# Performance work log

Hardware: AMD Instinct MI355X
Metric: run time of the kernel (lower is better)

The kernel has to match this reference:

```python
import jax, jax.numpy as jnp
import numpy as np

DIM = 1024
HEADS = 16
DIM_HEAD = 64


def setup_inputs() -> dict:
    key = jax.random.key(0)
    ks = jax.random.split(key, 6)
    b, n = 2, 2048
    x = jax.random.normal(ks[0], (b, n, DIM), dtype=jnp.float32)
    gamma = jnp.ones((DIM,), dtype=jnp.float32)
    w_qkv = jax.random.normal(ks[1], (DIM, 3 * HEADS * DIM_HEAD), dtype=jnp.float32) * (DIM ** -0.5)
    w_gates = jax.random.normal(ks[2], (DIM, HEADS), dtype=jnp.float32) * (DIM ** -0.5)
    b_gates = jnp.zeros((HEADS,), dtype=jnp.float32)
    w_out = jax.random.normal(ks[3], (HEADS * DIM_HEAD, DIM), dtype=jnp.float32) * ((HEADS * DIM_HEAD) ** -0.5)
    freqs = jax.random.uniform(ks[4], (DIM_HEAD // 2,), dtype=jnp.float32)
    return {"x": x, "gamma": gamma, "w_qkv": w_qkv, "w_gates": w_gates,
            "b_gates": b_gates, "w_out": w_out, "freqs": freqs}


def _rotate_half(t):
    # interleaved pairs: (x1, x2) -> (-x2, x1)
    tp = t.reshape(t.shape[:-1] + (t.shape[-1] // 2, 2))
    x1, x2 = tp[..., 0], tp[..., 1]
    return jnp.stack((-x2, x1), axis=-1).reshape(t.shape)


def reference(x, gamma, w_qkv, w_gates, b_gates, w_out, freqs):
    b, n, d = x.shape
    # RMSNorm variant: divide by L2 norm, scale by gamma * sqrt(dim)
    xn = x / jnp.linalg.norm(x, axis=-1, keepdims=True)
    xn = xn * gamma * (d ** 0.5)
    # QKV projection: (b, n, 3*H*D) -> q,k,v each (b, h, n, dh)
    qkv = xn @ w_qkv
    qkv = qkv.reshape(b, n, 3, HEADS, DIM_HEAD).transpose(2, 0, 3, 1, 4)
    q, k, v = qkv[0], qkv[1], qkv[2]
    # Inline RoPE (interleaved): freqs (n, dh)
    pos = jnp.arange(n, dtype=freqs.dtype)
    f = jnp.repeat(pos[:, None] * freqs[None, :], 2, axis=-1)  # (n, dh)
    cos_f, sin_f = jnp.cos(f), jnp.sin(f)
    q = q * cos_f + _rotate_half(q) * sin_f
    k = k * cos_f + _rotate_half(k) * sin_f
    # SDPA
    scale = DIM_HEAD ** -0.5
    scores = jnp.einsum('bhqd,bhkd->bhqk', q, k) * scale
    attn = jax.nn.softmax(scores, axis=-1)
    out = jnp.einsum('bhqk,bhkd->bhqd', attn, v)  # (b, h, n, dh)
    # per-head sigmoid gate from normalized input
    gates = xn @ w_gates + b_gates  # (b, n, h)
    out = out * jax.nn.sigmoid(gates.transpose(0, 2, 1))[..., None]
    # merge heads and output projection
    out = out.transpose(0, 2, 1, 3).reshape(b, n, HEADS * DIM_HEAD)
    return out @ w_out
```

## Files before the change

kernel.cpp:

```cpp
#include <hip/hip_runtime.h>

typedef __bf16 bf16_t;
typedef __bf16 bf16x8 __attribute__((ext_vector_type(8)));
typedef __bf16 bf16x4 __attribute__((ext_vector_type(4)));
typedef float f32x4 __attribute__((ext_vector_type(4)));

#define B_  2
#define N_  2048
#define D_  1024
#define H_  16
#define DH_ 64

#define QSCALE 0.18033688011112042f
#define NEGC  -11.541560327111707f

#if __has_builtin(__builtin_amdgcn_exp2f)
#define EXP2F(x) __builtin_amdgcn_exp2f(x)
#else
#define EXP2F(x) exp2f(x)
#endif

#define GLL16(g, l) __builtin_amdgcn_global_load_lds( \
    (const __attribute__((address_space(1))) void*)(g), \
    (__attribute__((address_space(3))) void*)(l), 16, 0, 0)

__device__ __forceinline__ int xcd_swizzle_id() {
  int id = blockIdx.y * gridDim.x + blockIdx.x;
  int cpx = (gridDim.x * gridDim.y) >> 3;
  return (id & 7) * cpx + (id >> 3);
}

__global__ __launch_bounds__(256) void k_rmsnorm_gates(const float* __restrict__ x,
    const float* __restrict__ gamma, const float* __restrict__ wg,
    const float* __restrict__ bg, bf16_t* __restrict__ xn, float* __restrict__ gsig) {
  int row = blockIdx.x;
  const float4* xr = (const float4*)(x + (size_t)row * D_);
  int tid = threadIdx.x;
  float4 v = xr[tid];
  float ss = v.x*v.x + v.y*v.y + v.z*v.z + v.w*v.w;
  #pragma unroll
  for (int off = 32; off > 0; off >>= 1) ss += __shfl_down(ss, off);
  __shared__ float red4[4];
  if ((tid & 63) == 0) red4[tid >> 6] = ss;
  __syncthreads();
  float scale = 32.0f * rsqrtf(red4[0] + red4[1] + red4[2] + red4[3]);
  float4 g = ((const float4*)gamma)[tid];
  bf16x4 o;
  o[0] = (bf16_t)(v.x * scale * g.x);
  o[1] = (bf16_t)(v.y * scale * g.y);
  o[2] = (bf16_t)(v.z * scale * g.z);
  o[3] = (bf16_t)(v.w * scale * g.w);
  *(bf16x4*)(xn + (size_t)row * D_ + tid * 4) = o;
  float xv[4] = {(float)o[0], (float)o[1], (float)o[2], (float)o[3]};
  float part[16];
  #pragma unroll
  for (int h = 0; h < 16; ++h) part[h] = 0.f;
  #pragma unroll
  for (int j = 0; j < 4; ++j) {
    const float4* wr = (const float4*)&wg[(size_t)(tid * 4 + j) * 16];
    #pragma unroll
    for (int q = 0; q < 4; ++q) {
      float4 w4 = wr[q];
      part[q * 4 + 0] += xv[j] * w4.x;
      part[q * 4 + 1] += xv[j] * w4.y;
      part[q * 4 + 2] += xv[j] * w4.z;
      part[q * 4 + 3] += xv[j] * w4.w;
    }
  }
  __shared__ float red[256][17];
  #pragma unroll
  for (int h = 0; h < 16; ++h) red[tid][h] = part[h];
  __syncthreads();
  int h = tid & 15, grp = tid >> 4;
  float s = 0.f;
  #pragma unroll
  for (int k = 0; k < 16; ++k) s += red[grp * 16 + k][h];
  __syncthreads();
  red[grp][h] = s;
  __syncthreads();
  if (tid < 16) {
    float acc = bg[tid];
    #pragma unroll
    for (int k = 0; k < 16; ++k) acc += red[k][tid];
    gsig[(size_t)row * 16 + tid] = 1.0f / (1.0f + __expf(-acc));
  }
}

__global__ __launch_bounds__(256) void k_transpose_cvt(const float* __restrict__ W,
    bf16_t* __restrict__ Wt, int R, int C) {
  __shared__ float tile[32][33];
  int c0 = blockIdx.x * 32, r0 = blockIdx.y * 32;
  int tx = threadIdx.x & 31, ty = threadIdx.x >> 5;
  #pragma unroll
  for (int i = 0; i < 4; ++i) {
    int r = ty + i * 8;
    tile[r][tx] = W[(size_t)(r0 + r) * C + c0 + tx];
  }
  __syncthreads();
  #pragma unroll
  for (int i = 0; i < 4; ++i) {
    int rr = ty + i * 8;
    Wt[(size_t)(c0 + rr) * R + r0 + tx] = (bf16_t)tile[tx][rr];
  }
}

template<bool OUT_BF16>
__global__ __launch_bounds__(256) void k_gemm_bt(const bf16_t* __restrict__ A,
    const bf16_t* __restrict__ Bt, void* __restrict__ Cp, int M, int N, int K) {
  constexpr int BK = 32;
  __shared__ __align__(16) bf16_t As[128 * BK];
  __shared__ __align__(16) bf16_t Bs[128 * BK];
  int tid = threadIdx.x, wave = tid >> 6, lane = tid & 63;
  int l16 = lane & 15, quad = lane >> 4;
  int swz = xcd_swizzle_id();
  int bxi = swz % gridDim.x, byi = swz / gridDim.x;
  int bm = bxi * 128, bn = byi * 128;
  int wm = (wave >> 1) * 64, wn = (wave & 1) * 64;
  int srow = wave * 32 + (lane >> 2);
  int scol = (lane & 3) * 8;
  const bf16_t* gA0 = &A [(size_t)(bm + srow)      * K + scol];
  const bf16_t* gA1 = &A [(size_t)(bm + srow + 16) * K + scol];
  const bf16_t* gB0 = &Bt[(size_t)(bn + srow)      * K + scol];
  const bf16_t* gB1 = &Bt[(size_t)(bn + srow + 16) * K + scol];
  bf16_t* lA0 = &As[(wave * 32)      * BK];
  bf16_t* lA1 = &As[(wave * 32 + 16) * BK];
  bf16_t* lB0 = &Bs[(wave * 32)      * BK];
  bf16_t* lB1 = &Bs[(wave * 32 + 16) * BK];
  f32x4 acc[4][4] = {};
  for (int k0 = 0; k0 < K; k0 += BK) {
    GLL16(gA0 + k0, lA0);
    GLL16(gA1 + k0, lA1);
    GLL16(gB0 + k0, lB0);
    GLL16(gB1 + k0, lB1);
    __syncthreads();
    bf16x8 af[4], bfr[4];
    #pragma unroll
    for (int t = 0; t < 4; ++t) {
      af[t]  = *(const bf16x8*)&As[(wm + t * 16 + l16) * BK + quad * 8];
      bfr[t] = *(const bf16x8*)&Bs[(wn + t * 16 + l16) * BK + quad * 8];
    }
    #pragma unroll
    for (int mt = 0; mt < 4; ++mt)
      #pragma unroll
      for (int nt = 0; nt < 4; ++nt)
        acc[mt][nt] = __builtin_amdgcn_mfma_f32_16x16x32_bf16(af[mt], bfr[nt], acc[mt][nt], 0, 0, 0);
    __syncthreads();
  }
  #pragma unroll
  for (int mt = 0; mt < 4; ++mt)
    #pragma unroll
    for (int nt = 0; nt < 4; ++nt)
      #pragma unroll
      for (int r = 0; r < 4; ++r) {
        int row = bm + wm + mt * 16 + quad * 4 + r;
        int col = bn + wn + nt * 16 + l16;
        float v = acc[mt][nt][r];
        if (OUT_BF16) ((bf16_t*)Cp)[(size_t)row * N + col] = (bf16_t)v;
        else          ((float*)Cp)[(size_t)row * N + col] = v;
      }
}

__global__ __launch_bounds__(256) void k_gemm_bt_n64(const bf16_t* __restrict__ A,
    const bf16_t* __restrict__ Bt, float* __restrict__ C, int M, int N, int K) {
  constexpr int BK = 32;
  __shared__ __align__(16) bf16_t As[128 * BK];
  __shared__ __align__(16) bf16_t Bs[64 * BK];
  int tid = threadIdx.x, wave = tid >> 6, lane = tid & 63;
  int l16 = lane & 15, quad = lane >> 4;
  int swz = xcd_swizzle_id();
  int bxi = swz % gridDim.x, byi = swz / gridDim.x;
  int bm = bxi * 128, bn = byi * 64;
  int wm = (wave >> 1) * 64, wn = (wave & 1) * 32;
  int srow = wave * 32 + (lane >> 2);
  int scol = (lane & 3) * 8;
  const bf16_t* gA0 = &A [(size_t)(bm + srow)      * K + scol];
  const bf16_t* gA1 = &A [(size_t)(bm + srow + 16) * K + scol];
  int srB = wave * 16 + (lane >> 2);
  const bf16_t* gB0 = &Bt[(size_t)(bn + srB) * K + scol];
  bf16_t* lA0 = &As[(wave * 32)      * BK];
  bf16_t* lA1 = &As[(wave * 32 + 16) * BK];
  bf16_t* lB0 = &Bs[(wave * 16)      * BK];
  f32x4 acc[4][2] = {};
  for (int k0 = 0; k0 < K; k0 += BK) {
    GLL16(gA0 + k0, lA0);
    GLL16(gA1 + k0, lA1);
    GLL16(gB0 + k0, lB0);
    __syncthreads();
    bf16x8 af[4], bfr[2];
    #pragma unroll
    for (int t = 0; t < 4; ++t)
      af[t]  = *(const bf16x8*)&As[(wm + t * 16 + l16) * BK + quad * 8];
    #pragma unroll
    for (int t = 0; t < 2; ++t)
      bfr[t] = *(const bf16x8*)&Bs[(wn + t * 16 + l16) * BK + quad * 8];
    #pragma unroll
    for (int mt = 0; mt < 4; ++mt)
      #pragma unroll
      for (int nt = 0; nt < 2; ++nt)
        acc[mt][nt] = __builtin_amdgcn_mfma_f32_16x16x32_bf16(af[mt], bfr[nt], acc[mt][nt], 0, 0, 0);
    __syncthreads();
  }
  #pragma unroll
  for (int mt = 0; mt < 4; ++mt)
    #pragma unroll
    for (int nt = 0; nt < 2; ++nt)
      #pragma unroll
      for (int r = 0; r < 4; ++r) {
        int row = bm + wm + mt * 16 + quad * 4 + r;
        int col = bn + wn + nt * 16 + l16;
        C[(size_t)row * N + col] = acc[mt][nt][r];
      }
}

__global__ __launch_bounds__(256) void k_rope(const bf16_t* __restrict__ qkvb,
    const float* __restrict__ freqs, bf16_t* __restrict__ Qb, bf16_t* __restrict__ Kb) {
  int row = blockIdx.x, b = row >> 11, n = row & 2047;
  __shared__ float cs[32], sn[32];
  int tid = threadIdx.x;
  if (tid < 32) { float f = (float)n * freqs[tid]; cs[tid] = cosf(f); sn[tid] = sinf(f); }
  __syncthreads();
  const bf16_t* src = qkvb + (size_t)row * 3072;
  int isK = tid >> 7;
  int t = tid & 127;
  int h = t >> 3, j8 = (t & 7) * 8;
  bf16x8 v = *(const bf16x8*)&src[isK * 1024 + h * 64 + j8];
  float qs = isK ? 1.0f : QSCALE;
  bf16x8 o;
  #pragma unroll
  for (int i = 0; i < 4; ++i) {
    int jj = (j8 >> 1) + i;
    float c = cs[jj], s = sn[jj];
    float v0 = (float)v[2 * i], v1 = (float)v[2 * i + 1];
    o[2 * i]     = (bf16_t)((v0 * c - v1 * s) * qs);
    o[2 * i + 1] = (bf16_t)((v1 * c + v0 * s) * qs);
  }
  bf16_t* dst = (isK ? Kb : Qb) + ((size_t)(b * H_ + h) * N_ + n) * DH_ + j8;
  *(bf16x8*)dst = o;
}

__global__ __launch_bounds__(256) void k_vtrans(const bf16_t* __restrict__ qkvb,
    bf16_t* __restrict__ Vb) {
  __shared__ bf16_t Vs[64][72];
  int bh = blockIdx.x, nt = blockIdx.y;
  int b = bh >> 4, h = bh & 15;
  int n0 = nt * 64;
  int tid = threadIdx.x;
  #pragma unroll
  for (int it = 0; it < 2; ++it) {
    int chunk = tid + 256 * it;
    int nl = chunk >> 3, c = (chunk & 7) * 8;
    *(bf16x8*)&Vs[nl][c] =
        *(const bf16x8*)&qkvb[(size_t)(b * N_ + n0 + nl) * 3072 + 2048 + h * 64 + c];
  }
  __syncthreads();
  #pragma unroll
  for (int it = 0; it < 2; ++it) {
    int chunk = tid + 256 * it;
    int d = chunk >> 3, nc = (chunk & 7) * 8;
    bf16x8 o;
    #pragma unroll
    for (int jj = 0; jj < 8; ++jj) o[jj] = Vs[nc + jj][d];
    *(bf16x8*)&Vb[((size_t)bh * DH_ + d) * N_ + n0 + nc] = o;
  }
}

__global__ __launch_bounds__(256) void k_flash(const bf16_t* __restrict__ Qb,
    const bf16_t* __restrict__ Kb, const bf16_t* __restrict__ Vb,
    const float* __restrict__ gsig, bf16_t* __restrict__ Ao) {
  __shared__ __align__(16) bf16_t Ks[2][64 * 72];
  __shared__ __align__(16) bf16_t Vt[2][64 * 72];
  __shared__ __align__(16) bf16_t Ps[4][32 * 72];
  int swz = xcd_swizzle_id();
  int qblk = swz & 15, bh = swz >> 4;
  int b = bh >> 4, h = bh & 15;
  int tid = threadIdx.x, wave = tid >> 6, lane = tid & 63;
  int l16 = lane & 15, quad = lane >> 4;
  int qw = qblk * 128 + wave * 32;
  const bf16_t* Qh = Qb + (size_t)bh * N_ * DH_;
  const bf16_t* Kh = Kb + (size_t)bh * N_ * DH_;
  const bf16_t* Vh = Vb + (size_t)bh * DH_ * N_;
  bf16_t* Pw = Ps[wave];
  bf16x8 qf[2][2];
  #pragma unroll
  for (int qt = 0; qt < 2; ++qt)
    #pragma unroll
    for (int hf = 0; hf < 2; ++hf)
      qf[qt][hf] = *(const bf16x8*)&Qh[(size_t)(qw + qt * 16 + l16) * DH_ + hf * 32 + quad * 8];
  bf16x8 onesf;
  #pragma unroll
  for (int i = 0; i < 8; ++i) onesf[i] = (bf16_t)1.0f;
  f32x4 accO[2][4] = {};
  f32x4 accL[2] = {};
  int sk = tid >> 3;
  int sc = (tid & 7) * 8;
  bf16x8 rk0 = *(const bf16x8*)&Kh[(size_t)sk * DH_ + sc];
  bf16x8 rk1 = *(const bf16x8*)&Kh[(size_t)(sk + 32) * DH_ + sc];
  bf16x8 rv0 = *(const bf16x8*)&Vh[(size_t)sk * N_ + sc];
  bf16x8 rv1 = *(const bf16x8*)&Vh[(size_t)(sk + 32) * N_ + sc];
  *(bf16x8*)&Ks[0][sk * 72 + sc]        = rk0;
  *(bf16x8*)&Ks[0][(sk + 32) * 72 + sc] = rk1;
  *(bf16x8*)&Vt[0][sk * 72 + sc]        = rv0;
  *(bf16x8*)&Vt[0][(sk + 32) * 72 + sc] = rv1;
  __syncthreads();
  const f32x4 zinit = {NEGC, NEGC, NEGC, NEGC};
  for (int k0 = 0; k0 < N_; k0 += 64) {
    int cur = (k0 >> 6) & 1;
    const bf16_t* Kc = Ks[cur];
    const bf16_t* Vc = Vt[cur];
    int kn = k0 + 64;
    if (kn < N_) {
      rk0 = *(const bf16x8*)&Kh[(size_t)(kn + sk) * DH_ + sc];
      rk1 = *(const bf16x8*)&Kh[(size_t)(kn + sk + 32) * DH_ + sc];
      rv0 = *(const bf16x8*)&Vh[(size_t)sk * N_ + kn + sc];
      rv1 = *(const bf16x8*)&Vh[(size_t)(sk + 32) * N_ + kn + sc];
    }
    f32x4 st[4][2];
    __builtin_amdgcn_s_setprio(1);
    #pragma unroll
    for (int kt = 0; kt < 4; ++kt) {
      bf16x8 kf0 = *(const bf16x8*)&Kc[(kt * 16 + l16) * 72 + quad * 8];
      bf16x8 kf1 = *(const bf16x8*)&Kc[(kt * 16 + l16) * 72 + 32 + quad * 8];
      #pragma unroll
      for (int qt = 0; qt < 2; ++qt) {
        f32x4 z = zinit;
        z = __builtin_amdgcn_mfma_f32_16x16x32_bf16(kf0, qf[qt][0], z, 0, 0, 0);
        z = __builtin_amdgcn_mfma_f32_16x16x32_bf16(kf1, qf[qt][1], z, 0, 0, 0);
        st[kt][qt] = z;
      }
    }
    __builtin_amdgcn_s_setprio(0);
    #pragma unroll
    for (int qt = 0; qt < 2; ++qt)
      #pragma unroll
      for (int kt = 0; kt < 4; ++kt) {
        bf16x4 pk;
        #pragma unroll
        for (int r = 0; r < 4; ++r)
          pk[r] = (bf16_t)EXP2F(st[kt][qt][r]);
        *(bf16x4*)&Pw[(qt * 16 + l16) * 72 + kt * 16 + quad * 4] = pk;
      }
    bf16x8 pf[2][2];
    #pragma unroll
    for (int qt = 0; qt < 2; ++qt)
      #pragma unroll
      for (int hf = 0; hf < 2; ++hf)
        pf[qt][hf] = *(const bf16x8*)&Pw[(qt * 16 + l16) * 72 + hf * 32 + quad * 8];
    __builtin_amdgcn_s_setprio(1);
    #pragma unroll
    for (int qt = 0; qt < 2; ++qt) {
      accL[qt] = __builtin_amdgcn_mfma_f32_16x16x32_bf16(pf[qt][0], onesf, accL[qt], 0, 0, 0);
      accL[qt] = __builtin_amdgcn_mfma_f32_16x16x32_bf16(pf[qt][1], onesf, accL[qt], 0, 0, 0);
    }
    #pragma unroll
    for (int dt = 0; dt < 4; ++dt)
      #pragma unroll
      for (int hf = 0; hf < 2; ++hf) {
        bf16x8 vf = *(const bf16x8*)&Vc[(dt * 16 + l16) * 72 + hf * 32 + quad * 8];
        #pragma unroll
        for (int qt = 0; qt < 2; ++qt)
          accO[qt][dt] = __builtin_amdgcn_mfma_f32_16x16x32_bf16(pf[qt][hf], vf, accO[qt][dt], 0, 0, 0);
      }
    __builtin_amdgcn_s_setprio(0);
    if (kn < N_) {
      int nb = cur ^ 1;
      *(bf16x8*)&Ks[nb][sk * 72 + sc]        = rk0;
      *(bf16x8*)&Ks[nb][(sk + 32) * 72 + sc] = rk1;
      *(bf16x8*)&Vt[nb][sk * 72 + sc]        = rv0;
      *(bf16x8*)&Vt[nb][(sk + 32) * 72 + sc] = rv1;
    }
    __syncthreads();
  }
  #pragma unroll
  for (int qt = 0; qt < 2; ++qt)
    #pragma unroll
    for (int r = 0; r < 4; ++r) {
      int q = qw + qt * 16 + quad * 4 + r;
      float g = gsig[((size_t)b * N_ + q) * H_ + h];
      float ginv = g / accL[qt][r];
      #pragma unroll
      for (int dt = 0; dt < 4; ++dt)
        Ao[((size_t)b * N_ + q) * (H_ * DH_) + h * DH_ + dt * 16 + l16] =
            (bf16_t)(accO[qt][dt][r] * ginv);
    }
}

extern "C" void kernel_launch(void* const* d_in, const int* in_sizes, int n_in,
                              void* d_out, int out_size, void* d_ws, size_t ws_size,
                              hipStream_t stream) {
  (void)in_sizes; (void)n_in; (void)out_size; (void)ws_size;
  const float* x      = (const float*)d_in[0];
  const float* gamma  = (const float*)d_in[1];
  const float* w_qkv  = (const float*)d_in[2];
  const float* w_gate = (const float*)d_in[3];
  const float* b_gate = (const float*)d_in[4];
  const float* w_out  = (const float*)d_in[5];
  const float* freqs  = (const float*)d_in[6];
  float* out = (float*)d_out;
  char* ws = (char*)d_ws;
  bf16_t* xn    = (bf16_t*)(ws);
  bf16_t* wqkvT = (bf16_t*)(ws + ((size_t)8  << 20));
  bf16_t* woutT = (bf16_t*)(ws + ((size_t)14 << 20));
  bf16_t* Qb    = (bf16_t*)(ws + ((size_t)16 << 20));
  bf16_t* Kb    = (bf16_t*)(ws + ((size_t)24 << 20));
  bf16_t* Vb    = (bf16_t*)(ws + ((size_t)32 << 20));
  float*  gsig  = (float*) (ws + ((size_t)40 << 20));
  bf16_t* attn  = (bf16_t*)(ws + ((size_t)41 << 20));
  bf16_t* qkvb  = (bf16_t*)(ws + ((size_t)49 << 20));

  k_transpose_cvt<<<dim3(3072 / 32, 1024 / 32), 256, 0, stream>>>(w_qkv, wqkvT, 1024, 3072);
  k_transpose_cvt<<<dim3(1024 / 32, 1024 / 32), 256, 0, stream>>>(w_out, woutT, 1024, 1024);
  k_rmsnorm_gates<<<4096, 256, 0, stream>>>(x, gamma, w_gate, b_gate, xn, gsig);
  k_gemm_bt<true><<<dim3(32, 24), 256, 0, stream>>>(xn, wqkvT, (void*)qkvb, 4096, 3072, 1024);
  k_rope<<<4096, 256, 0, stream>>>(qkvb, freqs, Qb, Kb);
  k_vtrans<<<dim3(32, 32), 256, 0, stream>>>(qkvb, Vb);
  k_flash<<<dim3(16, 32), 256, 0, stream>>>(Qb, Kb, Vb, gsig, attn);
  k_gemm_bt_n64<<<dim3(32, 16), 256, 0, stream>>>(attn, woutT, out, 4096, 1024, 1024);
}
```

Measured before the change: 239.2 us.

## Fuse RoPE and V transpose into QKV GEMM epilogue

Replaces the generic QKV GEMM plus separate rope and V-transpose kernels with one GEMM whose epilogue applies interleaved RoPE (using a lane shuffle to reach the partner element), scales Q, and writes Q/K in head-major layout and V transposed. A small kernel precomputes the cos/sin tables once per call. This removes the round-trip of the bf16 qkv intermediate through global memory and two launches. The price is scattered 2-byte stores for Q/K and 8-byte strided stores for V in the epilogue, which may coalesce poorly.

Result: no change. 242.4 us (+1.3%).

```diff
diff --git a/kernel.cpp b/kernel.cpp
--- a/kernel.cpp
+++ b/kernel.cpp
@@ -28,6 +28,15 @@
   int id = blockIdx.y * gridDim.x + blockIdx.x;
   int cpx = (gridDim.x * gridDim.y) >> 3;
   return (id & 7) * cpx + (id >> 3);
+}
+
+__global__ __launch_bounds__(256) void k_trig(const float* __restrict__ freqs,
+    float* __restrict__ tc, float* __restrict__ ts) {
+  int idx = blockIdx.x * 256 + threadIdx.x;
+  int n = idx >> 5, j = idx & 31;
+  float f = (float)n * freqs[j];
+  tc[idx] = cosf(f);
+  ts[idx] = sinf(f);
 }
 
 __global__ __launch_bounds__(256) void k_rmsnorm_gates(const float* __restrict__ x,
@@ -104,16 +113,17 @@
   }
 }
 
-template<bool OUT_BF16>
-__global__ __launch_bounds__(256) void k_gemm_bt(const bf16_t* __restrict__ A,
-    const bf16_t* __restrict__ Bt, void* __restrict__ Cp, int M, int N, int K) {
-  constexpr int BK = 32;
+__global__ __launch_bounds__(256) void k_gemm_qkv(const bf16_t* __restrict__ A,
+    const bf16_t* __restrict__ Bt, const float* __restrict__ tc,
+    const float* __restrict__ ts, bf16_t* __restrict__ Qb,
+    bf16_t* __restrict__ Kb, bf16_t* __restrict__ Vb) {
+  constexpr int BK = 32, K = 1024;
   __shared__ __align__(16) bf16_t As[128 * BK];
   __shared__ __align__(16) bf16_t Bs[128 * BK];
   int tid = threadIdx.x, wave = tid >> 6, lane = tid & 63;
   int l16 = lane & 15, quad = lane >> 4;
   int swz = xcd_swizzle_id();
-  int bxi = swz % gridDim.x, byi = swz / gridDim.x;
+  int bxi = swz % 32, byi = swz / 32;
   int bm = bxi * 128, bn = byi * 128;
   int wm = (wave >> 1) * 64, wn = (wave & 1) * 64;
   int srow = wave * 32 + (lane >> 2);
@@ -146,18 +156,43 @@
         acc[mt][nt] = __builtin_amdgcn_mfma_f32_16x16x32_bf16(af[mt], bfr[nt], acc[mt][nt], 0, 0, 0);
     __syncthreads();
   }
-  #pragma unroll
-  for (int mt = 0; mt < 4; ++mt)
-    #pragma unroll
-    for (int nt = 0; nt < 4; ++nt)
+  if (byi < 16) {
+    float qs = (byi < 8) ? QSCALE : 1.0f;
+    bf16_t* dst = (byi < 8) ? Qb : Kb;
+    #pragma unroll
+    for (int mt = 0; mt < 4; ++mt)
       #pragma unroll
       for (int r = 0; r < 4; ++r) {
         int row = bm + wm + mt * 16 + quad * 4 + r;
+        int b = row >> 11, n = row & 2047;
+        const float* cr = tc + n * 32;
+        const float* sr = ts + n * 32;
+        #pragma unroll
+        for (int nt = 0; nt < 4; ++nt) {
+          int col = bn + wn + nt * 16 + l16;
+          int h = (col >> 6) & 15, d = col & 63, j = d >> 1;
+          float val = acc[mt][nt][r];
+          float p = __shfl_xor(val, 1);
+          float c = cr[j], s = sr[j];
+          float o = (d & 1) ? (val * c + p * s) : (val * c - p * s);
+          dst[((size_t)(b * H_ + h) * N_ + n) * DH_ + d] = (bf16_t)(o * qs);
+        }
+      }
+  } else {
+    #pragma unroll
+    for (int mt = 0; mt < 4; ++mt)
+      #pragma unroll
+      for (int nt = 0; nt < 4; ++nt) {
+        int row0 = bm + wm + mt * 16 + quad * 4;
+        int b = row0 >> 11, n0 = row0 & 2047;
         int col = bn + wn + nt * 16 + l16;
-        float v = acc[mt][nt][r];
-        if (OUT_BF16) ((bf16_t*)Cp)[(size_t)row * N + col] = (bf16_t)v;
-        else          ((float*)Cp)[(size_t)row * N + col] = v;
-      }
+        int h = (col >> 6) & 15, d = col & 63;
+        bf16x4 pk;
+        #pragma unroll
+        for (int r = 0; r < 4; ++r) pk[r] = (bf16_t)acc[mt][nt][r];
+        *(bf16x4*)&Vb[((size_t)(b * H_ + h) * DH_ + d) * N_ + n0] = pk;
+      }
+  }
 }
 
 __global__ __launch_bounds__(256) void k_gemm_bt_n64(const bf16_t* __restrict__ A,
@@ -212,58 +247,6 @@
       }
 }
 
-__global__ __launch_bounds__(256) void k_rope(const bf16_t* __restrict__ qkvb,
-    const float* __restrict__ freqs, bf16_t* __restrict__ Qb, bf16_t* __restrict__ Kb) {
-  int row = blockIdx.x, b = row >> 11, n = row & 2047;
-  __shared__ float cs[32], sn[32];
-  int tid = threadIdx.x;
-  if (tid < 32) { float f = (float)n * freqs[tid]; cs[tid] = cosf(f); sn[tid] = sinf(f); }
-  __syncthreads();
-  const bf16_t* src = qkvb + (size_t)row * 3072;
-  int isK = tid >> 7;
-  int t = tid & 127;
-  int h = t >> 3, j8 = (t & 7) * 8;
-  bf16x8 v = *(const bf16x8*)&src[isK * 1024 + h * 64 + j8];
-  float qs = isK ? 1.0f : QSCALE;
-  bf16x8 o;
-  #pragma unroll
-  for (int i = 0; i < 4; ++i) {
-    int jj = (j8 >> 1) + i;
-    float c = cs[jj], s = sn[jj];
-    float v0 = (float)v[2 * i], v1 = (float)v[2 * i + 1];
-    o[2 * i]     = (bf16_t)((v0 * c - v1 * s) * qs);
-    o[2 * i + 1] = (bf16_t)((v1 * c + v0 * s) * qs);
-  }
-  bf16_t* dst = (isK ? Kb : Qb) + ((size_t)(b * H_ + h) * N_ + n) * DH_ + j8;
-  *(bf16x8*)dst = o;
-}
-
-__global__ __launch_bounds__(256) void k_vtrans(const bf16_t* __restrict__ qkvb,
-    bf16_t* __restrict__ Vb) {
-  __shared__ bf16_t Vs[64][72];
-  int bh = blockIdx.x, nt = blockIdx.y;
-  int b = bh >> 4, h = bh & 15;
-  int n0 = nt * 64;
-  int tid = threadIdx.x;
-  #pragma unroll
-  for (int it = 0; it < 2; ++it) {
-    int chunk = tid + 256 * it;
-    int nl = chunk >> 3, c = (chunk & 7) * 8;
-    *(bf16x8*)&Vs[nl][c] =
-        *(const bf16x8*)&qkvb[(size_t)(b * N_ + n0 + nl) * 3072 + 2048 + h * 64 + c];
-  }
-  __syncthreads();
-  #pragma unroll
-  for (int it = 0; it < 2; ++it) {
-    int chunk = tid + 256 * it;
-    int d = chunk >> 3, nc = (chunk & 7) * 8;
-    bf16x8 o;
-    #pragma unroll
-    for (int jj = 0; jj < 8; ++jj) o[jj] = Vs[nc + jj][d];
-    *(bf16x8*)&Vb[((size_t)bh * DH_ + d) * N_ + n0 + nc] = o;
-  }
-}
-
 __global__ __launch_bounds__(256) void k_flash(const bf16_t* __restrict__ Qb,
     const bf16_t* __restrict__ Kb, const bf16_t* __restrict__ Vb,
     const float* __restrict__ gsig, bf16_t* __restrict__ Ao) {
@@ -405,14 +388,14 @@
   bf16_t* Vb    = (bf16_t*)(ws + ((size_t)32 << 20));
   float*  gsig  = (float*) (ws + ((size_t)40 << 20));
   bf16_t* attn  = (bf16_t*)(ws + ((size_t)41 << 20));
-  bf16_t* qkvb  = (bf16_t*)(ws + ((size_t)49 << 20));
-
+  float*  trigc = (float*) (ws + ((size_t)49 << 20));
+  float*  trigs = (float*) (ws + ((size_t)50 << 20));
+
+  k_trig<<<256, 256, 0, stream>>>(freqs, trigc, trigs);
   k_transpose_cvt<<<dim3(3072 / 32, 1024 / 32), 256, 0, stream>>>(w_qkv, wqkvT, 1024, 3072);
   k_transpose_cvt<<<dim3(1024 / 32, 1024 / 32), 256, 0, stream>>>(w_out, woutT, 1024, 1024);
   k_rmsnorm_gates<<<4096, 256, 0, stream>>>(x, gamma, w_gate, b_gate, xn, gsig);
-  k_gemm_bt<true><<<dim3(32, 24), 256, 0, stream>>>(xn, wqkvT, (void*)qkvb, 4096, 3072, 1024);
-  k_rope<<<4096, 256, 0, stream>>>(qkvb, freqs, Qb, Kb);
-  k_vtrans<<<dim3(32, 32), 256, 0, stream>>>(qkvb, Vb);
+  k_gemm_qkv<<<dim3(32, 24), 256, 0, stream>>>(xn, wqkvT, trigc, trigs, Qb, Kb, Vb);
   k_flash<<<dim3(16, 32), 256, 0, stream>>>(Qb, Kb, Vb, gsig, attn);
   k_gemm_bt_n64<<<dim3(32, 16), 256, 0, stream>>>(attn, woutT, out, 4096, 1024, 1024);
 }
```
